# Kernel tuning notes

Hardware: AMD Instinct MI355X
Metric: run time of the kernel (lower is better)

## Reference

```python
import jax, jax.numpy as jnp
import numpy as np
import math

B, S, E = 4, 2048, 1024


def setup_inputs() -> dict:
    key = jax.random.key(0)
    ks = jax.random.split(key, 7)
    w_scale = 1.0 / math.sqrt(E)
    x = jax.random.normal(ks[0], (B, S, E), dtype=jnp.float32)
    Wq = jax.random.normal(ks[1], (E, E), dtype=jnp.float32) * w_scale
    bq = jax.random.normal(ks[2], (E,), dtype=jnp.float32) * 0.01
    Wk = jax.random.normal(ks[3], (E, E), dtype=jnp.float32) * w_scale
    bk = jax.random.normal(ks[4], (E,), dtype=jnp.float32) * 0.01
    Wv = jax.random.normal(ks[5], (E, E), dtype=jnp.float32) * w_scale
    bv = jax.random.normal(ks[6], (E,), dtype=jnp.float32) * 0.01
    # causal mask: True = attend, False = masked (mask == 0 -> -inf)
    mask = jnp.broadcast_to(jnp.tril(jnp.ones((S, S), dtype=bool)), (B, S, S))
    return {"x": x, "Wq": Wq, "bq": bq, "Wk": Wk, "bk": bk, "Wv": Wv, "bv": bv, "mask": mask}


def reference(x, Wq, bq, Wk, bk, Wv, bv, mask):
    # nn.Linear stores weight as [out, in]: y = x @ W.T + b
    Q = jnp.einsum("bse,oe->bso", x, Wq) + bq
    K = jnp.einsum("bse,oe->bso", x, Wk) + bk
    V = jnp.einsum("bse,oe->bso", x, Wv) + bv
    scale = math.sqrt(E)
    scores = jnp.einsum("bqe,bke->bqk", Q, K) / scale  # [B,S,S]
    scores = jnp.where(mask, scores, -jnp.inf)
    attn = jax.nn.softmax(scores, axis=-1)
    out = jnp.einsum("bqk,bke->bqe", attn, V)  # [B,S,E]
    return out
```

## Files before the change

### kernel.cpp

```cpp
#include <hip/hip_runtime.h>
#include <stdint.h>

typedef unsigned short u16;
typedef __attribute__((ext_vector_type(8))) short bf16x8;
typedef __attribute__((ext_vector_type(4))) float f32x4;

#define MFMA16(a, b, c) __builtin_amdgcn_mfma_f32_16x16x32_bf16((a), (b), (c), 0, 0, 0)

#define MASKVAL (-1.0e30f)

#define WAITV(N) asm volatile("s_waitcnt vmcnt(" #N ")" ::: "memory")
#define LGKM0()  asm volatile("s_waitcnt lgkmcnt(0)" ::: "memory")
#define SBAR()   __builtin_amdgcn_s_barrier()

__device__ __forceinline__ u16 f2bf(float f) {
  union { float f; uint32_t u; } v; v.f = f;
  uint32_t u = v.u;
  u += 0x7fffu + ((u >> 16) & 1u);
  return (u16)(u >> 16);
}
__device__ __forceinline__ void async16(const void* g, void* l) {
  __builtin_amdgcn_global_load_lds(
      (const __attribute__((address_space(1))) unsigned int*)g,
      (__attribute__((address_space(3))) unsigned int*)l, 16, 0, 0);
}

__global__ __launch_bounds__(256) void conv1_kernel(
    const float* __restrict__ x, u16* __restrict__ xbI)
{
  const int NX = 1 << 20;
  for (int i = blockIdx.x * 256 + threadIdx.x; i < NX; i += gridDim.x * 256) {
    const float* src = x + (size_t)i * 8;
    const int m = i >> 7, k8 = i & 127;
    float4 f0 = *(const float4*)src;
    float4 f1 = *(const float4*)(src + 4);
    ushort4 h0, h1;
    h0.x = f2bf(f0.x); h0.y = f2bf(f0.y); h0.z = f2bf(f0.z); h0.w = f2bf(f0.w);
    h1.x = f2bf(f1.x); h1.y = f2bf(f1.y); h1.z = f2bf(f1.z); h1.w = f2bf(f1.w);
    u16* dI = xbI + (size_t)m * 2048 + 1024 + k8 * 8;
    *(ushort4*)dI = h0; *(ushort4*)(dI + 4) = h1;
  }
}

__global__ __launch_bounds__(256) void conv2_kernel(
    const float* __restrict__ wq, const float* __restrict__ wk,
    const float* __restrict__ wv, u16* __restrict__ wb)
{
  const int NW = 1 << 17;
  const int total = NW * 3;
  for (int j = blockIdx.x * 256 + threadIdx.x; j < total; j += gridDim.x * 256) {
    const int wsel = j >> 17;
    const int jj = j & (NW - 1);
    const float* W = (wsel == 0) ? wq : (wsel == 1) ? wk : wv;
    const int zoff = (wsel == 0) ? 0 : (wsel == 1) ? (2 << 20) : (1 << 20);
    const float* src = W + (size_t)jj * 8;
    u16* dst = wb + zoff + jj * 8;
    float4 f0 = *(const float4*)src;
    float4 f1 = *(const float4*)(src + 4);
    ushort4 h0, h1;
    h0.x = f2bf(f0.x); h0.y = f2bf(f0.y); h0.z = f2bf(f0.z); h0.w = f2bf(f0.w);
    h1.x = f2bf(f1.x); h1.y = f2bf(f1.y); h1.z = f2bf(f1.z); h1.w = f2bf(f1.w);
    *(ushort4*)dst = h0;
    *(ushort4*)(dst + 4) = h1;
  }
}

__global__ __launch_bounds__(256) void gemm_kernel(
    const u16* __restrict__ xb,
    const u16* __restrict__ wb,
    const float* __restrict__ bq, const float* __restrict__ bk,
    const float* __restrict__ bv,
    u16* __restrict__ q_out, u16* __restrict__ vt_out, u16* __restrict__ k_out,
    u16* __restrict__ qcopy)
{
  __shared__ u16 lA[3][128 * 32];
  __shared__ u16 lB[3][128 * 32];

  const int flat = blockIdx.x;
  const int xcd = flat & 7, idx = flat >> 3;
  const int n_g = xcd * 3 + idx % 3;
  const int mm  = idx / 3;
  const int z   = n_g >> 3;
  const int m0 = mm * 128, n0 = (n_g & 7) * 128;

  const int tid = threadIdx.x, lane = tid & 63, w = tid >> 6;
  const int quad = lane >> 4, l15 = lane & 15;
  const int wr = (w >> 1) * 64, wc = (w & 1) * 64;

  const u16* wz = wb + ((size_t)z << 20);
  const float* bias = (z == 0) ? bq : (z == 1) ? bv : bk;

  const int sr  = lane >> 2;
  const int ssw = (lane >> 3) & 3;
  const int c16s = (lane & 3) ^ ssw;

  auto stageA = [&](int kk, int bbuf) {
    const int k0 = kk * 32;
#pragma unroll
    for (int i = 0; i < 2; ++i) {
      const int r = w * 32 + i * 16 + sr;
      async16(&xb[(size_t)(m0 + r) * 2048 + 1024 + k0 + c16s * 8],
              &lA[bbuf][w * 1024 + i * 512]);
    }
  };
  auto stageB = [&](int kk, int bbuf) {
    const int k0 = kk * 32;
#pragma unroll
    for (int i = 0; i < 2; ++i) {
      const int r = w * 32 + i * 16 + sr;
      async16(&wz[(size_t)(n0 + r) * 1024 + k0 + c16s * 8],
              &lB[bbuf][w * 1024 + i * 512]);
    }
  };

  f32x4 zero4 = {0.f, 0.f, 0.f, 0.f};
  f32x4 acc[4][4];
#pragma unroll
  for (int i = 0; i < 4; ++i)
#pragma unroll
    for (int j = 0; j < 4; ++j) acc[i][j] = zero4;

  stageA(0, 0); stageB(0, 0);
  stageA(1, 1); stageB(1, 1);

  const int fxor = (l15 >> 1) & 3;
  int cur = 0;
  for (int kk = 0; kk < 32; ++kk) {
    if (kk < 31) { WAITV(4); } else { WAITV(0); }
    SBAR();
    if (kk + 2 < 32) {
      int nx = cur + 2; if (nx >= 3) nx -= 3;
      stageA(kk + 2, nx);
      stageB(kk + 2, nx);
    }
    bf16x8 af[4], bw[4];
#pragma unroll
    for (int mf = 0; mf < 4; ++mf)
      af[mf] = *(const bf16x8*)
          &lA[cur][(wr + mf * 16 + l15) * 32 + (quad ^ fxor) * 8];
#pragma unroll
    for (int nf = 0; nf < 4; ++nf)
      bw[nf] = *(const bf16x8*)
          &lB[cur][(wc + nf * 16 + l15) * 32 + (quad ^ fxor) * 8];
    __builtin_amdgcn_s_setprio(1);
#pragma unroll
    for (int mf = 0; mf < 4; ++mf)
#pragma unroll
      for (int nf = 0; nf < 4; ++nf)
        acc[mf][nf] = MFMA16(af[mf], bw[nf], acc[mf][nf]);
    __builtin_amdgcn_s_setprio(0);
    cur = (cur == 2) ? 0 : cur + 1;
  }

  float bvv[4];
#pragma unroll
  for (int nf = 0; nf < 4; ++nf)
    bvv[nf] = bias[n0 + wc + nf * 16 + l15];

  if (z == 0) {
    const float qs = 0.03125f;
#pragma unroll
    for (int mf = 0; mf < 4; ++mf) {
#pragma unroll
      for (int nf = 0; nf < 4; ++nf) {
        const int n = n0 + wc + nf * 16 + l15;
#pragma unroll
        for (int r = 0; r < 4; ++r) {
          const int m = m0 + wr + mf * 16 + quad * 4 + r;
          const u16 qv = f2bf((acc[mf][nf][r] + bvv[nf]) * qs);
          q_out[(size_t)m * 2048 + n] = qv;
          const int s = m & 2047;
          if (s >= 1024)
            qcopy[((size_t)((m >> 11) << 10) + (s - 1024)) * 1024 + n] = qv;
        }
      }
    }
  } else if (z == 1) {
#pragma unroll
    for (int mf = 0; mf < 4; ++mf) {
      const int mbase = m0 + wr + mf * 16 + quad * 4;
      const int bb = mbase >> 11;
      const int ss = mbase & 2047;
#pragma unroll
      for (int nf = 0; nf < 4; ++nf) {
        const int n = n0 + wc + nf * 16 + l15;
        ushort4 pk;
        pk.x = f2bf(acc[mf][nf][0] + bvv[nf]);
        pk.y = f2bf(acc[mf][nf][1] + bvv[nf]);
        pk.z = f2bf(acc[mf][nf][2] + bvv[nf]);
        pk.w = f2bf(acc[mf][nf][3] + bvv[nf]);
        *(ushort4*)&vt_out[((size_t)bb << 21) + (size_t)n * 2048 + ss] = pk;
      }
    }
  } else {
#pragma unroll
    for (int mf = 0; mf < 4; ++mf) {
#pragma unroll
      for (int nf = 0; nf < 4; ++nf) {
        const int n = n0 + wc + nf * 16 + l15;
#pragma unroll
        for (int r = 0; r < 4; ++r) {
          const int m = m0 + wr + mf * 16 + quad * 4 + r;
          k_out[(size_t)m * 1024 + n] = f2bf(acc[mf][nf][r] + bvv[nf]);
        }
      }
    }
  }
}

__global__ __launch_bounds__(512) void attn_kernel(
    const u16* __restrict__ Q, const u16* __restrict__ K,
    const u16* __restrict__ VT, float* out,
    const u16* __restrict__ Qc, float* __restrict__ p1,
    float2* __restrict__ ml0, float2* __restrict__ ml1)
{
  constexpr int SLOT = 20480;
  __shared__ u16   ring[3][SLOT];
  __shared__ float sS[32 * 132];
  __shared__ u16   sP[32 * 136];
  __shared__ float sAlpha[32];
  __shared__ float sLinv[32];

  const int id = 95 - (int)blockIdx.x;
  const int b  = blockIdx.y;
  int t, it0, it1, mode;
  if (id < 32) { t = id; it0 = 0; it1 = t / 4 + 1; mode = 0; }
  else {
    const int p = id - 32;
    t = 32 + (p >> 1);
    const int full = t / 4 + 1;
    const int mid = full >> 1;
    if ((p & 1) == 0) { it0 = 0;   it1 = mid;  mode = 1; }
    else              { it0 = mid; it1 = full; mode = 2; }
  }
  const int q0 = t * 32;
  const int tid = threadIdx.x, lane = tid & 63, w = tid >> 6;
  const int quad = lane >> 4, l15 = lane & 15;
  const u16* Kb  = K  + ((size_t)b << 21);
  const u16* VTb = VT + ((size_t)b << 21);
  float* outb = out + ((size_t)b << 21);

  const u16* Qrow; int QS;
  if (mode == 0) { Qrow = Q + ((size_t)b << 22) + (size_t)q0 * 2048; QS = 2048; }
  else { Qrow = Qc + ((size_t)((b << 10) + (q0 - 1024))) * 1024;     QS = 1024; }

  const int sr = lane >> 4;
  const int sp = lane & 15;

  auto issueK = [&](int kv0, int e0, u16* slot) {
#pragma unroll
    for (int jj = 0; jj < 4; ++jj) {
      const int j = w * 4 + jj;
      const int r = j * 4 + sr;
      const int c16 = sp ^ (r & 15);
      async16(&Kb[(size_t)(kv0 + r) * 1024 + e0 + c16 * 8], slot + j * 512);
    }
  };
  auto issueV = [&](int kv0, int ck, u16* slot) {
#pragma unroll
    for (int jj = 0; jj < 4; ++jj) {
      const int j = w * 4 + jj;
      const int r = j * 4 + sr;
      const int c16 = sp ^ (r & 15);
      async16(&VTb[(size_t)(ck * 128 + r) * 2048 + kv0 + c16 * 8], slot + j * 512);
    }
  };
  auto issueQ = [&](int cq, u16* slot) {
    const int r = w * 4 + sr;
    const int c16 = sp ^ (r & 15);
    async16(&Qrow[(size_t)r * QS + cq * 128 + c16 * 8],
            slot + 16384 + w * 512);
  };

  f32x4 zero4 = {0.f, 0.f, 0.f, 0.f};
  f32x4 accO[8][2];
#pragma unroll
  for (int c = 0; c < 8; ++c)
#pragma unroll
    for (int i = 0; i < 2; ++i) accO[c][i] = zero4;

  float m_i = MASKVAL, l_i = 0.f;
  const int srow = tid >> 4, slane = tid & 15;

  issueK(it0 * 128, 0, ring[0]);   issueQ(0, ring[0]);
  issueK(it0 * 128, 128, ring[1]); issueQ(1, ring[1]);
  int sl = 0, sl2 = 2;

  for (int it = it0; it < it1; ++it) {
    const int kv0 = it * 128;

    f32x4 accS[2];
    accS[0] = zero4; accS[1] = zero4;

#pragma unroll
    for (int c = 0; c < 8; ++c) {
      if (c < 7) { WAITV(5); } else { WAITV(4); }
      SBAR();
      u16* dst = ring[sl2];
      if (c < 6)      { issueK(kv0, (c + 2) * 128, dst); issueQ(c + 2, dst); }
      else if (c == 6) issueV(kv0, 0, dst);
      else             issueV(kv0, 1, dst);
      const u16* bufK = ring[sl];
      const u16* bufQ = ring[sl] + 16384;
      __builtin_amdgcn_s_setprio(1);
#pragma unroll
      for (int ks = 0; ks < 4; ++ks) {
        const int cc = ks * 4 + quad;
        bf16x8 a0 = *(const bf16x8*)&bufQ[l15 * 128 + (cc ^ l15) * 8];
        bf16x8 a1 = *(const bf16x8*)&bufQ[(16 + l15) * 128 + (cc ^ l15) * 8];
        bf16x8 b0 = *(const bf16x8*)&bufK[(w * 16 + l15) * 128 + (cc ^ l15) * 8];
        accS[0] = MFMA16(a0, b0, accS[0]);
        accS[1] = MFMA16(a1, b0, accS[1]);
      }
      __builtin_amdgcn_s_setprio(0);
      sl  = (sl  == 2) ? 0 : sl  + 1;
      sl2 = (sl2 == 2) ? 0 : sl2 + 1;
    }

#pragma unroll
    for (int mf = 0; mf < 2; ++mf)
#pragma unroll
      for (int r = 0; r < 4; ++r) {
        const int row = mf * 16 + quad * 4 + r;
        const int col = w * 16 + l15;
        sS[row * 132 + col] = (kv0 + col <= q0 + row) ? accS[mf][r] : MASKVAL;
      }
    LGKM0();
    SBAR();

    {
      float v[8];
      float4 t0 = *(const float4*)&sS[srow * 132 + slane * 8 + 0];
      float4 t1 = *(const float4*)&sS[srow * 132 + slane * 8 + 4];
      v[0]=t0.x; v[1]=t0.y; v[2]=t0.z; v[3]=t0.w;
      v[4]=t1.x; v[5]=t1.y; v[6]=t1.z; v[7]=t1.w;
      float mx = v[0];
#pragma unroll
      for (int j = 1; j < 8; ++j) mx = fmaxf(mx, v[j]);
#pragma unroll
      for (int d = 1; d < 16; d <<= 1) mx = fmaxf(mx, __shfl_xor(mx, d, 64));
      const float mnew  = fmaxf(m_i, mx);
      const float alpha = __expf(m_i - mnew);
      float sum = 0.f;
      u16 pb[8];
#pragma unroll
      for (int j = 0; j < 8; ++j) {
        const float p = __expf(v[j] - mnew);
        pb[j] = f2bf(p);
        union { uint32_t u; float f; } pv; pv.u = ((uint32_t)pb[j]) << 16;
        sum += pv.f;
      }
      ushort4 pk0, pk1;
      pk0.x = pb[0]; pk0.y = pb[1]; pk0.z = pb[2]; pk0.w = pb[3];
      pk1.x = pb[4]; pk1.y = pb[5]; pk1.z = pb[6]; pk1.w = pb[7];
      *(ushort4*)&sP[srow * 136 + slane * 8 + 0] = pk0;
      *(ushort4*)&sP[srow * 136 + slane * 8 + 4] = pk1;
#pragma unroll
      for (int d = 1; d < 16; d <<= 1) sum += __shfl_xor(sum, d, 64);
      l_i = l_i * alpha + sum;
      m_i = mnew;
      if (slane == 0) sAlpha[srow] = alpha;
      if (mode == 0 && it == it1 - 1 && slane == 0) sLinv[srow] = 1.0f / l_i;
    }
    LGKM0();
    SBAR();

    float av[2][4];
#pragma unroll
    for (int mf = 0; mf < 2; ++mf)
#pragma unroll
      for (int r = 0; r < 4; ++r)
        av[mf][r] = sAlpha[mf * 16 + quad * 4 + r];
#pragma unroll
    for (int c = 0; c < 8; ++c)
#pragma unroll
      for (int mf = 0; mf < 2; ++mf)
#pragma unroll
        for (int r = 0; r < 4; ++r) accO[c][mf][r] *= av[mf][r];

    bf16x8 pf0[4], pf1[4];
#pragma unroll
    for (int ks = 0; ks < 4; ++ks) {
      const int cc = ks * 4 + quad;
      pf0[ks] = *(const bf16x8*)&sP[l15 * 136 + cc * 8];
      pf1[ks] = *(const bf16x8*)&sP[(16 + l15) * 136 + cc * 8];
    }

#pragma unroll
    for (int k = 0; k < 8; ++k) {
      if (k < 7)               { WAITV(4); }
      else if (it + 1 < it1)   { WAITV(5); }
      else                     { WAITV(0); }
      SBAR();
      u16* dst = ring[sl2];
      if (k < 6) issueV(kv0, k + 2, dst);
      else if (it + 1 < it1) {
        issueK(kv0 + 128, (k - 6) * 128, dst);
        issueQ(k - 6, dst);
      }
      const u16* bufV = ring[sl];
      __builtin_amdgcn_s_setprio(1);
#pragma unroll
      for (int ks = 0; ks < 4; ++ks) {
        const int cc = ks * 4 + quad;
        bf16x8 v0 = *(const bf16x8*)&bufV[(w * 16 + l15) * 128 + (cc ^ l15) * 8];
        accO[k][0] = MFMA16(pf0[ks], v0, accO[k][0]);
        accO[k][1] = MFMA16(pf1[ks], v0, accO[k][1]);
      }
      __builtin_amdgcn_s_setprio(0);
      sl  = (sl  == 2) ? 0 : sl  + 1;
      sl2 = (sl2 == 2) ? 0 : sl2 + 1;
    }
  }

  if (mode == 0) {
    float lv[2][4];
#pragma unroll
    for (int mf = 0; mf < 2; ++mf)
#pragma unroll
      for (int r = 0; r < 4; ++r)
        lv[mf][r] = sLinv[mf * 16 + quad * 4 + r];
#pragma unroll
    for (int c = 0; c < 8; ++c)
#pragma unroll
      for (int mf = 0; mf < 2; ++mf) {
        const int col = c * 128 + w * 16 + l15;
#pragma unroll
        for (int r = 0; r < 4; ++r) {
          const int row = q0 + mf * 16 + quad * 4 + r;
          outb[(size_t)row * 1024 + col] = accO[c][mf][r] * lv[mf][r];
        }
      }
  } else {
    const size_t rbase = (size_t)((b << 10) + (q0 - 1024));
#pragma unroll
    for (int c = 0; c < 8; ++c)
#pragma unroll
      for (int mf = 0; mf < 2; ++mf) {
        const int col = c * 128 + w * 16 + l15;
#pragma unroll
        for (int r = 0; r < 4; ++r) {
          const int row = mf * 16 + quad * 4 + r;
          if (mode == 1)
            outb[(size_t)(q0 + row) * 1024 + col] = accO[c][mf][r];
          else
            p1[(rbase + row) * 1024 + col] = accO[c][mf][r];
        }
      }
    if (slane == 0) {
      float2 v; v.x = m_i; v.y = l_i;
      if (mode == 1) ml0[rbase + srow] = v;
      else           ml1[rbase + srow] = v;
    }
  }
}

__global__ __launch_bounds__(256) void reduce_kernel(
    float* __restrict__ out, const float* __restrict__ p1,
    const float2* __restrict__ ml0, const float2* __restrict__ ml1)
{
  const int row = blockIdx.x;
  const int b = row >> 10, s = 1024 + (row & 1023);
  const float2 a = ml0[row], c = ml1[row];
  const float M  = fmaxf(a.x, c.x);
  const float w0 = __expf(a.x - M), w1 = __expf(c.x - M);
  const float inv = 1.0f / (a.y * w0 + c.y * w1);
  float* o = out + ((size_t)b << 21) + (size_t)s * 1024;
  const float* q1 = p1 + (size_t)row * 1024;
  const int j = threadIdx.x * 4;
  float4 v0 = *(const float4*)&o[j];
  float4 v1 = *(const float4*)&q1[j];
  float4 r;
  r.x = (v0.x * w0 + v1.x * w1) * inv;
  r.y = (v0.y * w0 + v1.y * w1) * inv;
  r.z = (v0.z * w0 + v1.z * w1) * inv;
  r.w = (v0.w * w0 + v1.w * w1) * inv;
  *(float4*)&o[j] = r;
}

extern "C" void kernel_launch(void* const* d_in, const int* in_sizes, int n_in,
                              void* d_out, int out_size, void* d_ws, size_t ws_size,
                              hipStream_t stream) {
  (void)in_sizes; (void)n_in; (void)out_size; (void)ws_size;
  const float* x  = (const float*)d_in[0];
  const float* Wq = (const float*)d_in[1];
  const float* bq = (const float*)d_in[2];
  const float* Wk = (const float*)d_in[3];
  const float* bk = (const float*)d_in[4];
  const float* Wv = (const float*)d_in[5];
  const float* bv = (const float*)d_in[6];
  char* xbuf = (char*)d_in[0];
  u16*    wb    = (u16*)xbuf;
  float2* ml0   = (float2*)(xbuf + (6u << 20));
  float2* ml1   = ml0 + 4096;
  float*  p1    = (float*)(xbuf + (8u << 20));
  u16*    qcopy = (u16*)(xbuf + (24u << 20));

  u16* qbuf = (u16*)d_out;
  u16* vtw  = (u16*)d_in[7];
  u16* kw   = (u16*)d_ws;

  conv1_kernel<<<dim3(2048), 256, 0, stream>>>(x, qbuf);
  conv2_kernel<<<dim3(512), 256, 0, stream>>>(Wq, Wk, Wv, wb);
  gemm_kernel<<<dim3(1536), 256, 0, stream>>>(qbuf, wb, bq, bk, bv,
                                              qbuf, vtw, kw, qcopy);
  attn_kernel<<<dim3(96, 4), 512, 0, stream>>>(qbuf, kw, vtw, (float*)d_out,
                                               qcopy, p1, ml0, ml1);
  reduce_kernel<<<dim3(4096), 256, 0, stream>>>((float*)d_out, p1, ml0, ml1);
}
```

Before: 432.4 us.

## Shrink attention LDS footprint and do softmax in registers for higher occupancy

Cuts the LDS ring slots from 128-wide to 64-wide chunks and moves Q into a separate double-buffered slab. The fp32 score staging buffer is replaced by in-register per-row softmax that uses cross-wave max/sum partials in small shared arrays. P fragments are now read from LDS inside the PV loop instead of being held in registers. The kernel also requests 4 blocks per CU via launch bounds, so the aim is more concurrent blocks and less LDS traffic. In exchange there are twice as many pipeline stages and barriers, and the register cap may cause spills.

```diff
diff --git a/kernel.cpp b/kernel.cpp
--- a/kernel.cpp
+++ b/kernel.cpp
@@ -208,18 +208,17 @@
   }
 }
 
-__global__ __launch_bounds__(512) void attn_kernel(
+__global__ __launch_bounds__(512, 4) void attn_kernel(
     const u16* __restrict__ Q, const u16* __restrict__ K,
     const u16* __restrict__ VT, float* out,
     const u16* __restrict__ Qc, float* __restrict__ p1,
     float2* __restrict__ ml0, float2* __restrict__ ml1)
 {
-  constexpr int SLOT = 20480;
-  __shared__ u16   ring[3][SLOT];
-  __shared__ float sS[32 * 132];
+  __shared__ u16   ring[3][8192];
+  __shared__ u16   qd[2][4096];
   __shared__ u16   sP[32 * 136];
-  __shared__ float sAlpha[32];
-  __shared__ float sLinv[32];
+  __shared__ float pmaxb[32][8];
+  __shared__ float psumb[32][8];
 
   const int id = 95 - (int)blockIdx.x;
   const int b  = blockIdx.y;
@@ -244,71 +243,79 @@
   if (mode == 0) { Qrow = Q + ((size_t)b << 22) + (size_t)q0 * 2048; QS = 2048; }
   else { Qrow = Qc + ((size_t)((b << 10) + (q0 - 1024))) * 1024;     QS = 1024; }
 
-  const int sr = lane >> 4;
-  const int sp = lane & 15;
-
-  auto issueK = [&](int kv0, int e0, u16* slot) {
-#pragma unroll
-    for (int jj = 0; jj < 4; ++jj) {
-      const int j = w * 4 + jj;
-      const int r = j * 4 + sr;
-      const int c16 = sp ^ (r & 15);
-      async16(&Kb[(size_t)(kv0 + r) * 1024 + e0 + c16 * 8], slot + j * 512);
+  const int sr8 = lane >> 3, g8 = lane & 7;
+  const int sr4 = lane >> 4, sp16 = lane & 15;
+
+  auto issueK = [&](int kv0_, int ec, u16* slot) {
+#pragma unroll
+    for (int jj = 0; jj < 2; ++jj) {
+      const int j = w * 2 + jj;
+      const int r = j * 8 + sr8;
+      async16(&Kb[(size_t)(kv0_ + r) * 1024 + ec * 64 + (g8 ^ sr8) * 8],
+              slot + j * 512);
     }
   };
-  auto issueV = [&](int kv0, int ck, u16* slot) {
-#pragma unroll
-    for (int jj = 0; jj < 4; ++jj) {
-      const int j = w * 4 + jj;
-      const int r = j * 4 + sr;
-      const int c16 = sp ^ (r & 15);
-      async16(&VTb[(size_t)(ck * 128 + r) * 2048 + kv0 + c16 * 8], slot + j * 512);
+  auto issueV = [&](int kv0_, int ec, int h, u16* slot) {
+#pragma unroll
+    for (int jj = 0; jj < 2; ++jj) {
+      const int j = w * 2 + jj;
+      const int r = j * 8 + sr8;
+      async16(&VTb[(size_t)(ec * 128 + r) * 2048 + kv0_ + h * 64 + (g8 ^ sr8) * 8],
+              slot + j * 512);
     }
   };
-  auto issueQ = [&](int cq, u16* slot) {
-    const int r = w * 4 + sr;
-    const int c16 = sp ^ (r & 15);
-    async16(&Qrow[(size_t)r * QS + cq * 128 + c16 * 8],
-            slot + 16384 + w * 512);
+  auto issueQslab = [&](int s, u16* dst) {
+    const int r = w * 4 + sr4;
+    async16(&Qrow[(size_t)r * QS + s * 128 + ((sp16 ^ (r & 15)) * 8)],
+            dst + w * 512);
   };
 
   f32x4 zero4 = {0.f, 0.f, 0.f, 0.f};
   f32x4 accO[8][2];
 #pragma unroll
-  for (int c = 0; c < 8; ++c)
-#pragma unroll
-    for (int i = 0; i < 2; ++i) accO[c][i] = zero4;
-
-  float m_i = MASKVAL, l_i = 0.f;
-  const int srow = tid >> 4, slane = tid & 15;
-
-  issueK(it0 * 128, 0, ring[0]);   issueQ(0, ring[0]);
-  issueK(it0 * 128, 128, ring[1]); issueQ(1, ring[1]);
+  for (int ec = 0; ec < 8; ++ec)
+#pragma unroll
+    for (int i = 0; i < 2; ++i) accO[ec][i] = zero4;
+
+  float m_i[2][4], l_i[2][4];
+#pragma unroll
+  for (int mf = 0; mf < 2; ++mf)
+#pragma unroll
+    for (int r = 0; r < 4; ++r) { m_i[mf][r] = MASKVAL; l_i[mf][r] = 0.f; }
+
+  issueQslab(0, qd[0]);
+  issueK(it0 * 128, 0, ring[0]);
+  issueK(it0 * 128, 1, ring[1]);
   int sl = 0, sl2 = 2;
 
   for (int it = it0; it < it1; ++it) {
     const int kv0 = it * 128;
+    const bool more = (it + 1 < it1);
 
     f32x4 accS[2];
     accS[0] = zero4; accS[1] = zero4;
 
 #pragma unroll
-    for (int c = 0; c < 8; ++c) {
-      if (c < 7) { WAITV(5); } else { WAITV(4); }
+    for (int c = 0; c < 16; ++c) {
+      if ((c & 1) && c < 15) { WAITV(3); } else { WAITV(2); }
       SBAR();
       u16* dst = ring[sl2];
-      if (c < 6)      { issueK(kv0, (c + 2) * 128, dst); issueQ(c + 2, dst); }
-      else if (c == 6) issueV(kv0, 0, dst);
-      else             issueV(kv0, 1, dst);
+      if (c <= 13) {
+        issueK(kv0, c + 2, dst);
+        if (!(c & 1)) issueQslab((c + 2) >> 1, qd[((c + 2) >> 1) & 1]);
+      } else if (c == 14) issueV(kv0, 0, 0, dst);
+      else                issueV(kv0, 0, 1, dst);
       const u16* bufK = ring[sl];
-      const u16* bufQ = ring[sl] + 16384;
+      const u16* bufQ = qd[(c >> 1) & 1];
+      const int eh = (c & 1) * 8;
       __builtin_amdgcn_s_setprio(1);
 #pragma unroll
-      for (int ks = 0; ks < 4; ++ks) {
-        const int cc = ks * 4 + quad;
-        bf16x8 a0 = *(const bf16x8*)&bufQ[l15 * 128 + (cc ^ l15) * 8];
-        bf16x8 a1 = *(const bf16x8*)&bufQ[(16 + l15) * 128 + (cc ^ l15) * 8];
-        bf16x8 b0 = *(const bf16x8*)&bufK[(w * 16 + l15) * 128 + (cc ^ l15) * 8];
+      for (int ks = 0; ks < 2; ++ks) {
+        const int gq = eh + ks * 4 + quad;
+        const int gk = ks * 4 + quad;
+        bf16x8 a0 = *(const bf16x8*)&bufQ[l15 * 128 + (gq ^ l15) * 8];
+        bf16x8 a1 = *(const bf16x8*)&bufQ[(16 + l15) * 128 + (gq ^ l15) * 8];
+        bf16x8 b0 = *(const bf16x8*)&bufK[(w * 16 + l15) * 64 + (gk ^ (l15 & 7)) * 8];
         accS[0] = MFMA16(a0, b0, accS[0]);
         accS[1] = MFMA16(a1, b0, accS[1]);
       }
@@ -317,95 +324,84 @@
       sl2 = (sl2 == 2) ? 0 : sl2 + 1;
     }
 
+    float alpha_[2][4];
+    const int colg = kv0 + w * 16 + l15;
 #pragma unroll
     for (int mf = 0; mf < 2; ++mf)
 #pragma unroll
       for (int r = 0; r < 4; ++r) {
         const int row = mf * 16 + quad * 4 + r;
-        const int col = w * 16 + l15;
-        sS[row * 132 + col] = (kv0 + col <= q0 + row) ? accS[mf][r] : MASKVAL;
+        accS[mf][r] = (colg <= q0 + row) ? accS[mf][r] : MASKVAL;
+        float mx = accS[mf][r];
+#pragma unroll
+        for (int d = 1; d < 16; d <<= 1) mx = fmaxf(mx, __shfl_xor(mx, d, 64));
+        if (l15 == 0) pmaxb[row][w] = mx;
       }
     LGKM0();
     SBAR();
-
-    {
-      float v[8];
-      float4 t0 = *(const float4*)&sS[srow * 132 + slane * 8 + 0];
-      float4 t1 = *(const float4*)&sS[srow * 132 + slane * 8 + 4];
-      v[0]=t0.x; v[1]=t0.y; v[2]=t0.z; v[3]=t0.w;
-      v[4]=t1.x; v[5]=t1.y; v[6]=t1.z; v[7]=t1.w;
-      float mx = v[0];
-#pragma unroll
-      for (int j = 1; j < 8; ++j) mx = fmaxf(mx, v[j]);
-#pragma unroll
-      for (int d = 1; d < 16; d <<= 1) mx = fmaxf(mx, __shfl_xor(mx, d, 64));
-      const float mnew  = fmaxf(m_i, mx);
-      const float alpha = __expf(m_i - mnew);
-      float sum = 0.f;
-      u16 pb[8];
-#pragma unroll
-      for (int j = 0; j < 8; ++j) {
-        const float p = __expf(v[j] - mnew);
-        pb[j] = f2bf(p);
-        union { uint32_t u; float f; } pv; pv.u = ((uint32_t)pb[j]) << 16;
-        sum += pv.f;
-      }
-      ushort4 pk0, pk1;
-      pk0.x = pb[0]; pk0.y = pb[1]; pk0.z = pb[2]; pk0.w = pb[3];
-      pk1.x = pb[4]; pk1.y = pb[5]; pk1.z = pb[6]; pk1.w = pb[7];
-      *(ushort4*)&sP[srow * 136 + slane * 8 + 0] = pk0;
-      *(ushort4*)&sP[srow * 136 + slane * 8 + 4] = pk1;
-#pragma unroll
-      for (int d = 1; d < 16; d <<= 1) sum += __shfl_xor(sum, d, 64);
-      l_i = l_i * alpha + sum;
-      m_i = mnew;
-      if (slane == 0) sAlpha[srow] = alpha;
-      if (mode == 0 && it == it1 - 1 && slane == 0) sLinv[srow] = 1.0f / l_i;
-    }
+#pragma unroll
+    for (int mf = 0; mf < 2; ++mf)
+#pragma unroll
+      for (int r = 0; r < 4; ++r) {
+        const int row = mf * 16 + quad * 4 + r;
+        float4 m0v = *(const float4*)&pmaxb[row][0];
+        float4 m1v = *(const float4*)&pmaxb[row][4];
+        const float mrow = fmaxf(fmaxf(fmaxf(m0v.x, m0v.y), fmaxf(m0v.z, m0v.w)),
+                                 fmaxf(fmaxf(m1v.x, m1v.y), fmaxf(m1v.z, m1v.w)));
+        const float mnew = fmaxf(m_i[mf][r], mrow);
+        alpha_[mf][r] = __expf(m_i[mf][r] - mnew);
+        m_i[mf][r] = mnew;
+        const float p = (colg <= q0 + row) ? __expf(accS[mf][r] - mnew) : 0.f;
+        const u16 pb = f2bf(p);
+        sP[row * 136 + w * 16 + l15] = pb;
+        union { uint32_t u; float f; } pv; pv.u = ((uint32_t)pb) << 16;
+        float s = pv.f;
+#pragma unroll
+        for (int d = 1; d < 16; d <<= 1) s += __shfl_xor(s, d, 64);
+        if (l15 == 0) psumb[row][w] = s;
+      }
     LGKM0();
     SBAR();
-
-    float av[2][4];
 #pragma unroll
     for (int mf = 0; mf < 2; ++mf)
 #pragma unroll
-      for (int r = 0; r < 4; ++r)
-        av[mf][r] = sAlpha[mf * 16 + quad * 4 + r];
-#pragma unroll
-    for (int c = 0; c < 8; ++c)
+      for (int r = 0; r < 4; ++r) {
+        const int row = mf * 16 + quad * 4 + r;
+        float4 s0v = *(const float4*)&psumb[row][0];
+        float4 s1v = *(const float4*)&psumb[row][4];
+        l_i[mf][r] = l_i[mf][r] * alpha_[mf][r]
+                   + ((s0v.x + s0v.y) + (s0v.z + s0v.w))
+                   + ((s1v.x + s1v.y) + (s1v.z + s1v.w));
+      }
+#pragma unroll
+    for (int ec = 0; ec < 8; ++ec)
 #pragma unroll
       for (int mf = 0; mf < 2; ++mf)
 #pragma unroll
-        for (int r = 0; r < 4; ++r) accO[c][mf][r] *= av[mf][r];
-
-    bf16x8 pf0[4], pf1[4];
-#pragma unroll
-    for (int ks = 0; ks < 4; ++ks) {
-      const int cc = ks * 4 + quad;
-      pf0[ks] = *(const bf16x8*)&sP[l15 * 136 + cc * 8];
-      pf1[ks] = *(const bf16x8*)&sP[(16 + l15) * 136 + cc * 8];
-    }
-
-#pragma unroll
-    for (int k = 0; k < 8; ++k) {
-      if (k < 7)               { WAITV(4); }
-      else if (it + 1 < it1)   { WAITV(5); }
-      else                     { WAITV(0); }
+        for (int r = 0; r < 4; ++r) accO[ec][mf][r] *= alpha_[mf][r];
+
+#pragma unroll
+    for (int k = 0; k < 16; ++k) {
+      if (k < 15)      { WAITV(2); }
+      else if (more)   { WAITV(3); }
+      else             { WAITV(0); }
       SBAR();
       u16* dst = ring[sl2];
-      if (k < 6) issueV(kv0, k + 2, dst);
-      else if (it + 1 < it1) {
-        issueK(kv0 + 128, (k - 6) * 128, dst);
-        issueQ(k - 6, dst);
-      }
+      if (k <= 13)      issueV(kv0, (k + 2) >> 1, (k + 2) & 1, dst);
+      else if (k == 14) { if (more) { issueQslab(0, qd[0]); issueK(kv0 + 128, 0, dst); } }
+      else              { if (more) issueK(kv0 + 128, 1, dst); }
       const u16* bufV = ring[sl];
+      const int ec = k >> 1, h = k & 1;
       __builtin_amdgcn_s_setprio(1);
 #pragma unroll
-      for (int ks = 0; ks < 4; ++ks) {
-        const int cc = ks * 4 + quad;
-        bf16x8 v0 = *(const bf16x8*)&bufV[(w * 16 + l15) * 128 + (cc ^ l15) * 8];
-        accO[k][0] = MFMA16(pf0[ks], v0, accO[k][0]);
-        accO[k][1] = MFMA16(pf1[ks], v0, accO[k][1]);
+      for (int ks = 0; ks < 2; ++ks) {
+        const int gp = h * 8 + ks * 4 + quad;
+        const int gv = ks * 4 + quad;
+        bf16x8 p0v = *(const bf16x8*)&sP[l15 * 136 + gp * 8];
+        bf16x8 p1v = *(const bf16x8*)&sP[(16 + l15) * 136 + gp * 8];
+        bf16x8 v0 = *(const bf16x8*)&bufV[(w * 16 + l15) * 64 + (gv ^ (l15 & 7)) * 8];
+        accO[ec][0] = MFMA16(p0v, v0, accO[ec][0]);
+        accO[ec][1] = MFMA16(p1v, v0, accO[ec][1]);
       }
       __builtin_amdgcn_s_setprio(0);
       sl  = (sl  == 2) ? 0 : sl  + 1;
@@ -414,43 +410,48 @@
   }
 
   if (mode == 0) {
-    float lv[2][4];
+    float linv[2][4];
 #pragma unroll
     for (int mf = 0; mf < 2; ++mf)
 #pragma unroll
-      for (int r = 0; r < 4; ++r)
-        lv[mf][r] = sLinv[mf * 16 + quad * 4 + r];
-#pragma unroll
-    for (int c = 0; c < 8; ++c)
+      for (int r = 0; r < 4; ++r) linv[mf][r] = 1.0f / l_i[mf][r];
+#pragma unroll
+    for (int ec = 0; ec < 8; ++ec)
 #pragma unroll
       for (int mf = 0; mf < 2; ++mf) {
-        const int col = c * 128 + w * 16 + l15;
+        const int col = ec * 128 + w * 16 + l15;
 #pragma unroll
         for (int r = 0; r < 4; ++r) {
           const int row = q0 + mf * 16 + quad * 4 + r;
-          outb[(size_t)row * 1024 + col] = accO[c][mf][r] * lv[mf][r];
+          outb[(size_t)row * 1024 + col] = accO[ec][mf][r] * linv[mf][r];
         }
       }
   } else {
     const size_t rbase = (size_t)((b << 10) + (q0 - 1024));
 #pragma unroll
-    for (int c = 0; c < 8; ++c)
+    for (int ec = 0; ec < 8; ++ec)
 #pragma unroll
       for (int mf = 0; mf < 2; ++mf) {
-        const int col = c * 128 + w * 16 + l15;
+        const int col = ec * 128 + w * 16 + l15;
 #pragma unroll
         for (int r = 0; r < 4; ++r) {
           const int row = mf * 16 + quad * 4 + r;
           if (mode == 1)
-            outb[(size_t)(q0 + row) * 1024 + col] = accO[c][mf][r];
+            outb[(size_t)(q0 + row) * 1024 + col] = accO[ec][mf][r];
           else
-            p1[(rbase + row) * 1024 + col] = accO[c][mf][r];
+            p1[(rbase + row) * 1024 + col] = accO[ec][mf][r];
         }
       }
-    if (slane == 0) {
-      float2 v; v.x = m_i; v.y = l_i;
-      if (mode == 1) ml0[rbase + srow] = v;
-      else           ml1[rbase + srow] = v;
+    if (w == 0 && l15 == 0) {
+#pragma unroll
+      for (int mf = 0; mf < 2; ++mf)
+#pragma unroll
+        for (int r = 0; r < 4; ++r) {
+          const int row = mf * 16 + quad * 4 + r;
+          float2 v; v.x = m_i[mf][r]; v.y = l_i[mf][r];
+          if (mode == 1) ml0[rbase + row] = v;
+          else           ml1[rbase + row] = v;
+        }
     }
   }
 }
```

New measurement: 668.9 us. 1.55x slower.
